# Optimization experiments

Measured on AMD Instinct MI355X. Metric: run time of the kernel, lower is better.

Reference implementation:

```python
import jax, jax.numpy as jnp
import numpy as np

LN_EPS = 1e-5


def _layernorm_c(x, g, b):
    # x: (B, C, H, W); LayerNorm over channel dim (torch permutes to channels-last)
    m = x.mean(axis=1, keepdims=True)
    v = ((x - m) ** 2).mean(axis=1, keepdims=True)
    xn = (x - m) / jnp.sqrt(v + LN_EPS)
    return xn * g[None, :, None, None] + b[None, :, None, None]


def _conv1x1(x, w, b):
    # w: (O, C) equivalent of Conv2d kernel_size=1
    return jnp.einsum('oc,bchw->bohw', w, x) + b[None, :, None, None]


def _rel_indices(lw):
    # matches torch: indices (x,y) for x in range(lw) for y in range(lw);
    # torch indexes the (2*lw-1, 2*lw-1) table with NEGATIVE distances (python wrap),
    # which equals modulo (2*lw-1).
    pos = np.stack(np.meshgrid(np.arange(lw), np.arange(lw), indexing='ij'), -1).reshape(-1, 2)
    rel = (pos[None, :, :] - pos[:, None, :]) % (2 * lw - 1)
    return rel[..., 0], rel[..., 1]


def setup_inputs() -> dict:
    key = jax.random.key(0)
    ks = jax.random.split(key, 8)
    B, N, D, H, DFF, LW = 1, 240, 256, 8, 2048, 20
    src = jax.random.normal(ks[0], (B, D, N, N), dtype=jnp.float32)
    valid = 220  # last window block fully padded -> exercises full-mask reset path
    pad1d = jnp.arange(N) >= valid
    padding_mask = (pad1d[:, None] | pad1d[None, :])[None, None]  # (B,1,N,N) bool
    s = 0.02
    return {
        'src': src,
        'padding_mask': padding_mask,
        'qkv_w': jax.random.normal(ks[1], (3 * D, D), dtype=jnp.float32) * s,
        'qkv_b': jnp.zeros((3 * D,), jnp.float32),
        'out_w': jax.random.normal(ks[2], (D, D), dtype=jnp.float32) * s,
        'out_b': jnp.zeros((D,), jnp.float32),
        'lin1_w': jax.random.normal(ks[3], (DFF, D), dtype=jnp.float32) * s,
        'lin1_b': jnp.zeros((DFF,), jnp.float32),
        'lin2_w': jax.random.normal(ks[4], (D, DFF), dtype=jnp.float32) * s,
        'lin2_b': jnp.zeros((D,), jnp.float32),
        'n1_g': jnp.ones((D,), jnp.float32),
        'n1_b': jnp.zeros((D,), jnp.float32),
        'n2_g': jnp.ones((D,), jnp.float32),
        'n2_b': jnp.zeros((D,), jnp.float32),
        'rel_bias': jax.random.normal(ks[5], (2 * LW - 1, 2 * LW - 1, H), dtype=jnp.float32) * 0.02,
    }


def reference(src, padding_mask, qkv_w, qkv_b, out_w, out_b, lin1_w, lin1_b,
              lin2_w, lin2_b, n1_g, n1_b, n2_g, n2_b, rel_bias):
    B, D, N, _ = src.shape
    H = rel_bias.shape[-1]
    LW = (rel_bias.shape[0] + 1) // 2
    nw = N // LW           # shift_offset=0, N % LW == 0 -> no spatial padding
    F = LW * LW            # eff_attn_field
    hd = D // H
    scaling = float(hd) ** -0.5

    # pre-norm
    src2 = _layernorm_c(src, n1_g, n1_b)

    # window partition: (B,D,N,N) -> (B*nw*nw, D, LW, LW)
    pm = src2.reshape(B, D, nw, LW, nw, LW).transpose(0, 2, 4, 1, 3, 5)
    pm = pm.reshape(B * nw * nw, D, LW, LW)

    # key padding mask per window: (B*nw*nw, F)
    kpm = padding_mask[:, 0].reshape(B, nw, LW, nw, LW).transpose(0, 1, 3, 2, 4)
    kpm = kpm.reshape(B * nw * nw, F)
    full = kpm.all(axis=-1)                      # fully padded windows
    kpm = kpm & (~full)[:, None]                 # index_fill_(False) equivalent

    # qkv (1x1 conv) + heads
    qkv = _conv1x1(pm, qkv_w, qkv_b)             # (eb, 3D, LW, LW)
    q, k, v = jnp.split(qkv, 3, axis=1)
    eb = q.shape[0]
    q = (q * scaling).reshape(eb, H, hd, F)
    k = k.reshape(eb, H, hd, F)
    v = v.reshape(eb, H, hd, F)

    attn = jnp.einsum('bhdi,bhdj->bhij', q, k)   # (eb, H, F, F)
    attn = jnp.where(kpm[:, None, None, :], -jnp.inf, attn)
    r0, r1 = _rel_indices(LW)
    rel = rel_bias[r0, r1]                       # (F, F, H)
    attn = attn + jnp.transpose(rel, (2, 0, 1))[None]
    attn = jax.nn.softmax(attn, axis=-1)

    out = jnp.einsum('bhij,bhdj->bhdi', attn, v).reshape(eb, D, LW, LW)
    out = _conv1x1(out, out_w, out_b)

    # window merge: (B*nw*nw, D, LW, LW) -> (B, D, N, N)
    out = out.reshape(B, nw, nw, D, LW, LW).transpose(0, 3, 1, 4, 2, 5).reshape(B, D, N, N)

    src = src + out  # dropout1 = identity (eval)

    # FFN
    s2 = _layernorm_c(src, n2_g, n2_b)
    s2 = _conv1x1(jax.nn.relu(_conv1x1(s2, lin1_w, lin1_b)), lin2_w, lin2_b)
    src = src + s2   # dropout2 = identity (eval)

    src = jnp.where(padding_mask, 0.0, src)
    return src
```

## Files before the change

kernel.cpp:

```cpp
#include <hip/hip_runtime.h>
#include <hip/hip_bf16.h>
#include <math.h>

typedef unsigned short u16;
typedef unsigned int   u32;
typedef __attribute__((ext_vector_type(8))) short bf16x8;
typedef __attribute__((ext_vector_type(4))) float f32x4;
typedef __attribute__((ext_vector_type(16))) float f32x16;
typedef __attribute__((ext_vector_type(4))) u32 u32x4;

#define NSIDE  240
#define NPIX   57600
#define DMODEL 256
#define NHEAD  8
#define HDIM   32
#define LWIN   20
#define NWIN   12
#define FF     400
#define DFFN   2048
#define BTAB   39
#define LOG2E  1.4426950408889634f
#define QSCALE 0.2550773933046f

#define OFF_QKVW  0u
#define OFF_OUTW  393216u
#define OFF_W1    524288u
#define OFF_W2    1572864u
#define OFF_FLAG  2621440u
#define OFF_WANY  2621504u
#define OFF_WMASK 2622080u
#define OFF_NM    2629568u
#define OFF_A     2687488u
#define OFF_B     32178688u

__device__ __forceinline__ float bf2f(u16 u){
  union { float f; u32 i; } v; v.i = ((u32)u) << 16; return v.f;
}
__device__ __forceinline__ float bflo(u32 u){
  union { float f; u32 i; } v; v.i = u << 16; return v.f;
}
__device__ __forceinline__ float bfhi(u32 u){
  union { float f; u32 i; } v; v.i = u & 0xffff0000u; return v.f;
}
__device__ __forceinline__ u16 f2bf(float f){
  union { float f; u32 i; } v; v.f = f;
  u32 r = v.i + 0x7fffu + ((v.i >> 16) & 1u);
  return (u16)(r >> 16);
}
__device__ __forceinline__ u32 pkbf(float a, float b){
  float2 f2; f2.x = a; f2.y = b;
  __hip_bfloat162 h = __float22bfloat162_rn(f2);
  union { __hip_bfloat162 h; u32 u; } c; c.h = h; return c.u;
}
__device__ __forceinline__ void gload16(const void* g, void* l){
  __builtin_amdgcn_global_load_lds((const __attribute__((address_space(1))) u32*)g,
                                   (__attribute__((address_space(3))) u32*)l, 16, 0, 0);
}
__device__ __forceinline__ void gload16nt(const void* g, void* l){
  __builtin_amdgcn_global_load_lds((const __attribute__((address_space(1))) u32*)g,
                                   (__attribute__((address_space(3))) u32*)l, 16, 0, 2);
}

__global__ void cvt_kernel(const float* __restrict__ in, u16* __restrict__ out, int n){
  int i = blockIdx.x * 256 + threadIdx.x;
  if (i < n) out[i] = f2bf(in[i]);
}
__global__ void cvt_w1T(const float* __restrict__ in, u16* __restrict__ out){
  int i = blockIdx.x * 256 + threadIdx.x;
  int f = i >> 8, k = i & 255;
  int lane = (f & 15) | (((k >> 3) & 3) << 4);
  size_t dst = ((size_t)((f >> 4) * 8 + (k >> 5)) * 64 + lane) * 8 + (k & 7);
  out[dst] = f2bf(in[i]);
}
__global__ void cvt_w2T(const float* __restrict__ in, u16* __restrict__ out){
  int i = blockIdx.x * 256 + threadIdx.x;
  int o = i >> 11, f = i & 2047;
  int lane = (o & 15) | (((f >> 3) & 3) << 4);
  size_t dst = ((size_t)((o >> 4) * 64 + (f >> 5)) * 64 + lane) * 8 + (f & 7);
  out[dst] = f2bf(in[i]);
}

__global__ void zero_flag(int* __restrict__ flag){ *flag = 0; }
__global__ void detect_mask(const unsigned char* __restrict__ m, int* __restrict__ flag){
  int p = blockIdx.x * 256 + threadIdx.x;
  int i = p / NSIDE, j = p - i * NSIDE;
  int a = (m[p] != 0), b = (m[j * NSIDE + i] != 0);
  unsigned long long ball = __ballot(a != b);
  if ((threadIdx.x & 63) == 0 && ball) atomicOr(flag, 1);
}
__global__ void norm_mask(const void* __restrict__ m, const int* __restrict__ flag,
                          unsigned char* __restrict__ nm){
  int p = blockIdx.x * 256 + threadIdx.x;
  int v;
  if (*flag) v = (((const int*)m)[p] != 0);
  else       v = (((const unsigned char*)m)[p] != 0);
  nm[p] = (unsigned char)v;
}

__global__ void wmask_kernel(const unsigned char* __restrict__ nm,
                             u32* __restrict__ wmask, int* __restrict__ wany){
  int w = blockIdx.x;
  int wi = w / NWIN, wj = w % NWIN;
  __shared__ u32 bits[13];
  __shared__ int cnt;
  int t = threadIdx.x;
  if (t < 13) bits[t] = 0;
  if (t == 0) cnt = 0;
  __syncthreads();
  if (t < FF){
    int pj = (wi * LWIN + t / LWIN) * NSIDE + wj * LWIN + (t % LWIN);
    if (nm[pj]){ atomicOr(&bits[t >> 5], 1u << (t & 31)); atomicAdd(&cnt, 1); }
  }
  __syncthreads();
  int full = (cnt == FF);
  if (t < 13) wmask[w * 13 + t] = full ? 0u : bits[t];
  if (t == 0) wany[w] = (cnt > 0 && !full) ? 1 : 0;
}

__global__ __launch_bounds__(256) void ln_kernel(const float* __restrict__ x,
                          const float* __restrict__ g, const float* __restrict__ b,
                          u16* __restrict__ out){
  int p = blockIdx.x * 256 + threadIdx.x;
  float s = 0.f, s2 = 0.f;
  for (int c = 0; c < DMODEL; c++){
    float v = x[c * NPIX + p];
    s += v; s2 += v * v;
  }
  float m = s * (1.f / DMODEL);
  float var = s2 * (1.f / DMODEL) - m * m;
  float inv = rsqrtf(var + 1e-5f);
  u16* orow = out + (size_t)p * DMODEL;
  for (int c0 = 0; c0 < DMODEL; c0 += 8){
    u32 wq[4];
    #pragma unroll
    for (int q = 0; q < 4; q++){
      int c = c0 + 2 * q;
      float v0 = (x[c * NPIX + p] - m) * inv * g[c] + b[c];
      float v1 = (x[(c + 1) * NPIX + p] - m) * inv * g[c + 1] + b[c + 1];
      wq[q] = pkbf(v0, v1);
    }
    uint4 st; st.x = wq[0]; st.y = wq[1]; st.z = wq[2]; st.w = wq[3];
    *(uint4*)&orow[c0] = st;
  }
}

template<int EPI, int XHM>
__global__ __launch_bounds__(256) void gemm_nt(const u16* __restrict__ W,
    const u16* __restrict__ Xt, const float* __restrict__ bias,
    const float* __restrict__ res, void* __restrict__ outp, int M){
  __shared__ u16 SM[128 * 128];
  u16* Ws = SM;
  u16* Xs = SM + 8192;
  int t = threadIdx.x, wv = t >> 6, ln = t & 63;
  int n0 = blockIdx.x * 128, m0 = blockIdx.y * 128;
  int wr = wv >> 1, wc = wv & 1;
  f32x4 acc[4][4];
  #pragma unroll
  for (int r = 0; r < 4; r++)
    #pragma unroll
    for (int c = 0; c < 4; c++) acc[r][c] = (f32x4)0.f;
  const char* Wb = (const char*)W;
  const char* Xb = (const char*)Xt;
  for (int k0 = 0; k0 < 256; k0 += 64){
    #pragma unroll
    for (int i = 0; i < 4; i++){
      int cb = i * 256 + wv * 64;
      int idx = cb + ln;
      int row = idx >> 3, cc = idx & 7;
      int cc2 = cc ^ (row & 7);
      gload16(Wb + (size_t)(m0 + row) * 512 + k0 * 2 + (cc2 << 4), (char*)Ws + cb * 16);
      if (XHM){
        int head = (k0 >> 5) + (cc2 >> 2);
        gload16(Xb + ((size_t)head * NPIX + n0 + row) * 64 + ((cc2 & 3) << 4),
                (char*)Xs + cb * 16);
      } else {
        gload16(Xb + (size_t)(n0 + row) * 512 + k0 * 2 + (cc2 << 4), (char*)Xs + cb * 16);
      }
    }
    __syncthreads();
    #pragma unroll
    for (int kk = 0; kk < 64; kk += 32){
      int kidx = kk + (ln >> 4) * 8;
      int swz = (ln & 7) << 3;
      bf16x8 af[4], bfr[4];
      #pragma unroll
      for (int r = 0; r < 4; r++){
        int row = wr * 64 + r * 16 + (ln & 15);
        af[r] = *(const bf16x8*)&Ws[row * 64 + (kidx ^ swz)];
      }
      #pragma unroll
      for (int c = 0; c < 4; c++){
        int row = wc * 64 + c * 16 + (ln & 15);
        bfr[c] = *(const bf16x8*)&Xs[row * 64 + (kidx ^ swz)];
      }
      #pragma unroll
      for (int r = 0; r < 4; r++)
        #pragma unroll
        for (int c = 0; c < 4; c++)
          acc[r][c] = __builtin_amdgcn_mfma_f32_16x16x32_bf16(af[r], bfr[c], acc[r][c], 0, 0, 0);
    }
    __syncthreads();
  }
  if (EPI == 2){
    float sc = (m0 < 256) ? QSCALE : 1.0f;
    #pragma unroll
    for (int r = 0; r < 4; r++){
      int mo0 = wr * 64 + r * 16 + (ln >> 4) * 4;
      f32x4 bv = *(const f32x4*)&bias[m0 + mo0];
      #pragma unroll
      for (int c = 0; c < 4; c++){
        int no = wc * 64 + c * 16 + (ln & 15);
        uint2 pk;
        pk.x = pkbf((acc[r][c][0] + bv[0]) * sc, (acc[r][c][1] + bv[1]) * sc);
        pk.y = pkbf((acc[r][c][2] + bv[2]) * sc, (acc[r][c][3] + bv[3]) * sc);
        *(uint2*)&SM[no * 128 + mo0] = pk;
      }
    }
    __syncthreads();
    u16* ob = (u16*)outp;
    int plane8 = (m0 >> 8) * 8 + ((m0 & 255) >> 5);
    #pragma unroll
    for (int it = 0; it < 8; it++){
      int idx = t + it * 256;
      int pr = idx >> 4, ch = idx & 15;
      int hl = ch >> 2;
      int off = (ch & 3) * 8;
      uint4 v = *(const uint4*)&SM[pr * 128 + ch * 8];
      *(uint4*)&ob[((size_t)(plane8 + hl) * NPIX + n0 + pr) * 32 + off] = v;
    }
  } else {
    #pragma unroll
    for (int r = 0; r < 4; r++){
      int mo0 = m0 + wr * 64 + r * 16 + (ln >> 4) * 4;
      f32x4 bv = *(const f32x4*)&bias[mo0];
      #pragma unroll
      for (int c = 0; c < 4; c++){
        int no = n0 + wc * 64 + c * 16 + (ln & 15);
        #pragma unroll
        for (int q = 0; q < 4; q++){
          float v = acc[r][c][q] + bv[q];
          size_t oi = (size_t)(mo0 + q) * NPIX + no;
          ((float*)outp)[oi] = v + res[oi];
        }
      }
    }
  }
}

__global__ __launch_bounds__(256, 2) void attn_kernel(
    const u16* __restrict__ qkvP, const float* __restrict__ relb,
    const u32* __restrict__ wmask, const int* __restrict__ wany,
    u16* __restrict__ out)
{
  __shared__ u16 Ks[400 * 32];
  __shared__ u16 Vs[32 * 420];
  __shared__ float bs[BTAB * BTAB];
  int bid = blockIdx.x;
  int h = bid & 7, w = bid >> 3;
  int wi = w / NWIN, wj = w % NWIN;
  int t = threadIdx.x, wv = t >> 6, ln = t & 63;
  const char* kpl = (const char*)qkvP + (size_t)(8 + h) * NPIX * 64;
  const u16*  vpl = qkvP + (size_t)(16 + h) * NPIX * 32;
  const u16*  qpl = qkvP + (size_t)h * NPIX * 32;
  for (int e = t; e < BTAB * BTAB; e += 256){
    int a = e / BTAB, b = e - a * BTAB;
    int r0 = a + 20; if (r0 >= BTAB) r0 -= BTAB;
    int r1 = b + 20; if (r1 >= BTAB) r1 -= BTAB;
    bs[e] = LOG2E * relb[(r0 * BTAB + r1) * NHEAD + h];
  }
  #pragma unroll
  for (int it = 0; it < 7; it++){
    int base = it * 256 + wv * 64;
    if (base < 1600){
      int idx = base + ln;
      int j = idx >> 2, c = idx & 3;
      int pj = (wi * LWIN + j / LWIN) * NSIDE + wj * LWIN + (j % LWIN);
      gload16nt(kpl + (size_t)pj * 64 + ((c ^ (j & 3)) << 4), (char*)Ks + base * 16);
    }
  }
  for (int it = 0; it < 7; it++){
    int idx = t + it * 256;
    int j = idx >> 2, c = idx & 3;
    if (j >= 416) break;
    int d0 = c * 8;
    if (j < FF){
      int pj = (wi * LWIN + j / LWIN) * NSIDE + wj * LWIN + (j % LWIN);
      u32x4 vv = __builtin_nontemporal_load((const u32x4*)&vpl[(size_t)pj * 32 + c * 8]);
      #pragma unroll
      for (int q = 0; q < 4; q++){
        Vs[(d0 + 2 * q) * 420 + j]     = (u16)vv[q];
        Vs[(d0 + 2 * q + 1) * 420 + j] = (u16)(vv[q] >> 16);
      }
    } else {
      #pragma unroll
      for (int q = 0; q < 4; q++){
        Vs[(d0 + 2 * q) * 420 + j]     = 0;
        Vs[(d0 + 2 * q + 1) * 420 + j] = 0;
      }
    }
  }
  __syncthreads();
  int lane31 = ln & 31, hi = ln >> 5;
  int anym = wany[w];
  for (int it8 = wv; it8 < 13; it8 += 4){
    int i = it8 * 32 + lane31;
    int ic = i < FF ? i : FF - 1;
    int xi = ic / LWIN, yi = ic - xi * LWIN;
    int pi = (wi * LWIN + xi) * NSIDE + wj * LWIN + yi;
    int Coff = (19 - xi) * BTAB + (19 - yi);
    bf16x8 qf0 = __builtin_nontemporal_load((const bf16x8*)&qpl[(size_t)pi * 32 + hi * 8]);
    bf16x8 qf1 = __builtin_nontemporal_load((const bf16x8*)&qpl[(size_t)pi * 32 + 16 + hi * 8]);
    float m = -3e38f, lsum = 0.f;
    f32x16 o;
    #pragma unroll
    for (int r = 0; r < 16; r++) o[r] = 0.f;
    for (int jt = 0; jt < 13; jt++){
      f32x16 acc;
      int jbase = jt * 32 + 4 * hi;
      #pragma unroll
      for (int r = 0; r < 16; r++){
        int j = jbase + (r & 3) + 8 * (r >> 2);
        int jc2 = j < FF ? j : 0;
        int xj = jc2 / LWIN;
        int yj = jc2 - xj * LWIN;
        float bv = bs[xj * BTAB + yj + Coff];
        acc[r] = (j < FF) ? bv : -1e30f;
      }
      int jb0 = jt * 32 + lane31;
      int jrc = jb0 < FF ? jb0 : FF - 1;
      const char* kb = (const char*)Ks + jrc * 64;
      bf16x8 kf0 = *(const bf16x8*)(kb + ((hi ^ (jrc & 3)) << 4));
      bf16x8 kf1 = *(const bf16x8*)(kb + (((2 + hi) ^ (jrc & 3)) << 4));
      acc = __builtin_amdgcn_mfma_f32_32x32x16_bf16(kf0, qf0, acc, 0, 0, 0);
      acc = __builtin_amdgcn_mfma_f32_32x32x16_bf16(kf1, qf1, acc, 0, 0, 0);
      if (anym){
        u32 mb = wmask[w * 13 + jt];
        if (mb){
          #pragma unroll
          for (int r = 0; r < 16; r++){
            int jb = (r & 3) + 8 * (r >> 2) + 4 * hi;
            if ((mb >> jb) & 1) acc[r] = -1e30f;
          }
        }
      }
      float tm = acc[0];
      #pragma unroll
      for (int r = 1; r < 16; r++) tm = fmaxf(tm, acc[r]);
      tm = fmaxf(tm, __shfl_xor(tm, 32));
      if (tm > m + 6.f){
        float sc = exp2f(m - tm);
        lsum *= sc;
        #pragma unroll
        for (int r = 0; r < 16; r++) o[r] *= sc;
        m = tm;
      }
      float ls = 0.f;
      #pragma unroll
      for (int r = 0; r < 16; r++){ float pv = exp2f(acc[r] - m); acc[r] = pv; ls += pv; }
      lsum += ls;
      u32 x01 = pkbf(acc[0], acc[1]), x23 = pkbf(acc[2], acc[3]);
      u32 x45 = pkbf(acc[4], acc[5]), x67 = pkbf(acc[6], acc[7]);
      u32 y01 = __shfl_xor(x01, 32), y23 = __shfl_xor(x23, 32);
      u32 y45 = __shfl_xor(x45, 32), y67 = __shfl_xor(x67, 32);
      union { u32 u[4]; bf16x8 v; } f0;
      f0.u[0] = hi ? y45 : x01; f0.u[1] = hi ? y67 : x23;
      f0.u[2] = hi ? x45 : y01; f0.u[3] = hi ? x67 : y23;
      bf16x8 vf0 = *(const bf16x8*)&Vs[lane31 * 420 + jt * 32 + hi * 8];
      o = __builtin_amdgcn_mfma_f32_32x32x16_bf16(vf0, f0.v, o, 0, 0, 0);
      if (jt < 12){
        u32 x89 = pkbf(acc[8], acc[9]),   xab = pkbf(acc[10], acc[11]);
        u32 xcd2 = pkbf(acc[12], acc[13]), xef = pkbf(acc[14], acc[15]);
        u32 y89 = __shfl_xor(x89, 32), yab = __shfl_xor(xab, 32);
        u32 ycd = __shfl_xor(xcd2, 32), yef = __shfl_xor(xef, 32);
        union { u32 u[4]; bf16x8 v; } f1;
        f1.u[0] = hi ? ycd : x89; f1.u[1] = hi ? yef : xab;
        f1.u[2] = hi ? xcd2 : y89; f1.u[3] = hi ? xef : yab;
        bf16x8 vf1 = *(const bf16x8*)&Vs[lane31 * 420 + jt * 32 + 16 + hi * 8];
        o = __builtin_amdgcn_mfma_f32_32x32x16_bf16(vf1, f1.v, o, 0, 0, 0);
      }
    }
    lsum += __shfl_xor(lsum, 32);
    if (i < FF){
      float linv = 1.f / lsum;
      u16* orow = out + ((size_t)h * NPIX + pi) * 32;
      #pragma unroll
      for (int g = 0; g < 4; g++){
        int ch0 = g * 8 + hi * 4;
        uint2 st;
        st.x = pkbf(o[g * 4 + 0] * linv, o[g * 4 + 1] * linv);
        st.y = pkbf(o[g * 4 + 2] * linv, o[g * 4 + 3] * linv);
        *(uint2*)&orow[ch0] = st;
      }
    }
  }
}

__global__ __launch_bounds__(256, 3) void ffn_kernel(const u16* __restrict__ xt,
    const u16* __restrict__ w1T, const u16* __restrict__ w2T,
    const float* __restrict__ b1, const float* __restrict__ b2,
    const float* __restrict__ resid, const unsigned char* __restrict__ pmask,
    float* __restrict__ out){
  __shared__ u16 Xs[64 * 256];
  __shared__ u16 Hs[64 * 136];
  int t = threadIdx.x, wv = t >> 6, ln = t & 63;
  int q4 = ln >> 4, l15 = ln & 15;
  int p0 = blockIdx.x * 64;
  const char* xb = (const char*)xt + (size_t)p0 * 512;
  #pragma unroll
  for (int it = 0; it < 8; it++){
    int cb = it * 256 + wv * 64;
    int idx = cb + ln;
    int row = idx >> 5, cc = idx & 31;
    gload16(xb + row * 512 + ((cc << 4) ^ ((row & 7) << 4)), (char*)Xs + cb * 16);
  }
  f32x4 acc[4][4];
  #pragma unroll
  for (int r = 0; r < 4; r++)
    #pragma unroll
    for (int c = 0; c < 4; c++) acc[r][c] = (f32x4)0.f;
  int swx = (ln & 7) << 3;
  __syncthreads();
  for (int fc = 0; fc < DFFN; fc += 128){
    f32x4 ha[2][4];
    #pragma unroll
    for (int ft = 0; ft < 2; ft++)
      #pragma unroll
      for (int c = 0; c < 4; c++) ha[ft][c] = (f32x4)0.f;
    const u16* w1f = w1T + ((size_t)((fc >> 4) + wv * 2) * 8 * 64 + ln) * 8;
    #pragma unroll
    for (int kg = 0; kg < 8; kg++){
      bf16x8 aw0 = *(const bf16x8*)(w1f + (size_t)kg * 512);
      bf16x8 aw1 = *(const bf16x8*)(w1f + (size_t)(8 + kg) * 512);
      #pragma unroll
      for (int c = 0; c < 4; c++){
        int p = c * 16 + l15;
        bf16x8 bx = *(const bf16x8*)&Xs[p * 256 + ((kg * 32 + q4 * 8) ^ swx)];
        ha[0][c] = __builtin_amdgcn_mfma_f32_16x16x32_bf16(aw0, bx, ha[0][c], 0, 0, 0);
        ha[1][c] = __builtin_amdgcn_mfma_f32_16x16x32_bf16(aw1, bx, ha[1][c], 0, 0, 0);
      }
    }
    __syncthreads();
    #pragma unroll
    for (int ft = 0; ft < 2; ft++){
      int f0 = wv * 32 + ft * 16 + q4 * 4;
      f32x4 bv1 = *(const f32x4*)&b1[fc + f0];
      #pragma unroll
      for (int c = 0; c < 4; c++){
        int p = c * 16 + l15;
        uint2 pk;
        pk.x = pkbf(fmaxf(ha[ft][c][0] + bv1[0], 0.f), fmaxf(ha[ft][c][1] + bv1[1], 0.f));
        pk.y = pkbf(fmaxf(ha[ft][c][2] + bv1[2], 0.f), fmaxf(ha[ft][c][3] + bv1[3], 0.f));
        *(uint2*)&Hs[p * 136 + f0] = pk;
      }
    }
    __syncthreads();
    #pragma unroll
    for (int kk2 = 0; kk2 < 4; kk2++){
      bf16x8 a2[4], hb[4];
      #pragma unroll
      for (int r = 0; r < 4; r++)
        a2[r] = *(const bf16x8*)(w2T + ((size_t)((wv * 4 + r) * 64 + (fc >> 5) + kk2) * 64 + ln) * 8);
      #pragma unroll
      for (int c = 0; c < 4; c++)
        hb[c] = *(const bf16x8*)&Hs[(c * 16 + l15) * 136 + kk2 * 32 + q4 * 8];
      #pragma unroll
      for (int r = 0; r < 4; r++)
        #pragma unroll
        for (int c = 0; c < 4; c++)
          acc[r][c] = __builtin_amdgcn_mfma_f32_16x16x32_bf16(a2[r], hb[c], acc[r][c], 0, 0, 0);
    }
  }
  #pragma unroll
  for (int r = 0; r < 4; r++){
    int o0 = wv * 64 + r * 16 + q4 * 4;
    f32x4 bv = *(const f32x4*)&b2[o0];
    #pragma unroll
    for (int c = 0; c < 4; c++){
      int p = p0 + c * 16 + l15;
      int msk = pmask[p];
      #pragma unroll
      for (int q = 0; q < 4; q++){
        size_t oi = (size_t)(o0 + q) * NPIX + p;
        float v = acc[r][c][q] + bv[q] + resid[oi];
        out[oi] = msk ? 0.f : v;
      }
    }
  }
}

extern "C" void kernel_launch(void* const* d_in, const int* in_sizes, int n_in,
                              void* d_out, int out_size, void* d_ws, size_t ws_size,
                              hipStream_t stream){
  const float* src    = (const float*)d_in[0];
  const void*  pmraw  = d_in[1];
  const float* qkv_w  = (const float*)d_in[2];
  const float* qkv_b  = (const float*)d_in[3];
  const float* out_w  = (const float*)d_in[4];
  const float* out_b  = (const float*)d_in[5];
  const float* lin1_w = (const float*)d_in[6];
  const float* lin1_b = (const float*)d_in[7];
  const float* lin2_w = (const float*)d_in[8];
  const float* lin2_b = (const float*)d_in[9];
  const float* n1_g   = (const float*)d_in[10];
  const float* n1_b   = (const float*)d_in[11];
  const float* n2_g   = (const float*)d_in[12];
  const float* n2_b   = (const float*)d_in[13];
  const float* relb   = (const float*)d_in[14];

  char* ws = (char*)d_ws;
  u16* qkvw_bf = (u16*)(ws + OFF_QKVW);
  u16* outw_bf = (u16*)(ws + OFF_OUTW);
  u16* w1_fr   = (u16*)(ws + OFF_W1);
  u16* w2_fr   = (u16*)(ws + OFF_W2);
  int* flag    = (int*)(ws + OFF_FLAG);
  int* wany    = (int*)(ws + OFF_WANY);
  u32* wmaskp  = (u32*)(ws + OFF_WMASK);
  unsigned char* nm = (unsigned char*)(ws + OFF_NM);
  u16* bufA    = (u16*)(ws + OFF_A);
  u16* qkvP    = (u16*)(ws + OFF_B);
  float* x1    = (float*)(ws + OFF_B);

  cvt_kernel<<<768,  256, 0, stream>>>(qkv_w,  qkvw_bf, 768 * 256);
  cvt_kernel<<<256,  256, 0, stream>>>(out_w,  outw_bf, 256 * 256);
  cvt_w1T<<<2048, 256, 0, stream>>>(lin1_w, w1_fr);
  cvt_w2T<<<2048, 256, 0, stream>>>(lin2_w, w2_fr);
  zero_flag<<<1, 1, 0, stream>>>(flag);
  detect_mask<<<225, 256, 0, stream>>>((const unsigned char*)pmraw, flag);
  norm_mask<<<225, 256, 0, stream>>>(pmraw, flag, nm);
  wmask_kernel<<<144, 512, 0, stream>>>(nm, wmaskp, wany);

  ln_kernel<<<225, 256, 0, stream>>>(src, n1_g, n1_b, bufA);
  gemm_nt<2, 0><<<dim3(450, 6), 256, 0, stream>>>(qkvw_bf, bufA, qkv_b, nullptr,
                                                  (void*)qkvP, 768);
  attn_kernel<<<1152, 256, 0, stream>>>(qkvP, relb, wmaskp, wany, bufA);
  gemm_nt<1, 1><<<dim3(450, 2), 256, 0, stream>>>(outw_bf, bufA, out_b, src,
                                                  (void*)x1, 256);
  ln_kernel<<<225, 256, 0, stream>>>(x1, n2_g, n2_b, bufA);
  ffn_kernel<<<900, 256, 0, stream>>>(bufA, w1_fr, w2_fr, lin1_b, lin2_b, x1, nm,
                                      (float*)d_out);
}
```

Before: 550.8 us.

## Keep FFN input in registers and double-buffer hidden tile to drop a barrier

The first FFN GEMM now has each wave own a 16-pixel slice and hold its X fragments in registers. Each wave computes all 128 hidden features for its pixels, where before each wave computed 32 features across all 64 pixels. The shared-memory arena is reused: X is staged once, then the space becomes a double-buffered hidden tile, so one __syncthreads per chunk is removed and LDS use drops. In exchange, every wave now reads the whole 128-feature W1 chunk from global memory (four times the per-wave weight traffic), and register pressure rises.

```diff
diff --git a/kernel.cpp b/kernel.cpp
--- a/kernel.cpp
+++ b/kernel.cpp
@@ -21,6 +21,7 @@
 #define BTAB   39
 #define LOG2E  1.4426950408889634f
 #define QSCALE 0.2550773933046f
+#define HSTR   136
 
 #define OFF_QKVW  0u
 #define OFF_OUTW  393216u
@@ -400,8 +401,7 @@
     const float* __restrict__ b1, const float* __restrict__ b2,
     const float* __restrict__ resid, const unsigned char* __restrict__ pmask,
     float* __restrict__ out){
-  __shared__ u16 Xs[64 * 256];
-  __shared__ u16 Hs[64 * 136];
+  __shared__ u16 SM[17408];
   int t = threadIdx.x, wv = t >> 6, ln = t & 63;
   int q4 = ln >> 4, l15 = ln & 15;
   int p0 = blockIdx.x * 64;
@@ -411,47 +411,44 @@
     int cb = it * 256 + wv * 64;
     int idx = cb + ln;
     int row = idx >> 5, cc = idx & 31;
-    gload16(xb + row * 512 + ((cc << 4) ^ ((row & 7) << 4)), (char*)Xs + cb * 16);
-  }
+    gload16(xb + row * 512 + ((cc << 4) ^ ((row & 7) << 4)), (char*)SM + cb * 16);
+  }
+  __syncthreads();
+  int swx = (ln & 7) << 3;
+  bf16x8 bxr[8];
+  #pragma unroll
+  for (int kg = 0; kg < 8; kg++)
+    bxr[kg] = *(const bf16x8*)&SM[(wv * 16 + l15) * 256 + ((kg * 32 + q4 * 8) ^ swx)];
   f32x4 acc[4][4];
   #pragma unroll
   for (int r = 0; r < 4; r++)
     #pragma unroll
     for (int c = 0; c < 4; c++) acc[r][c] = (f32x4)0.f;
-  int swx = (ln & 7) << 3;
   __syncthreads();
-  for (int fc = 0; fc < DFFN; fc += 128){
-    f32x4 ha[2][4];
-    #pragma unroll
-    for (int ft = 0; ft < 2; ft++)
-      #pragma unroll
-      for (int c = 0; c < 4; c++) ha[ft][c] = (f32x4)0.f;
-    const u16* w1f = w1T + ((size_t)((fc >> 4) + wv * 2) * 8 * 64 + ln) * 8;
+  int cur = 0;
+  for (int fc = 0; fc < DFFN; fc += 128, cur ^= 1){
+    u16* Hc = SM + cur * 8704;
+    f32x4 ha[8];
+    #pragma unroll
+    for (int ft = 0; ft < 8; ft++) ha[ft] = (f32x4)0.f;
+    const u16* w1f = w1T + ((size_t)(fc >> 4) * 512 + ln) * 8;
     #pragma unroll
     for (int kg = 0; kg < 8; kg++){
-      bf16x8 aw0 = *(const bf16x8*)(w1f + (size_t)kg * 512);
-      bf16x8 aw1 = *(const bf16x8*)(w1f + (size_t)(8 + kg) * 512);
-      #pragma unroll
-      for (int c = 0; c < 4; c++){
-        int p = c * 16 + l15;
-        bf16x8 bx = *(const bf16x8*)&Xs[p * 256 + ((kg * 32 + q4 * 8) ^ swx)];
-        ha[0][c] = __builtin_amdgcn_mfma_f32_16x16x32_bf16(aw0, bx, ha[0][c], 0, 0, 0);
-        ha[1][c] = __builtin_amdgcn_mfma_f32_16x16x32_bf16(aw1, bx, ha[1][c], 0, 0, 0);
-      }
-    }
-    __syncthreads();
-    #pragma unroll
-    for (int ft = 0; ft < 2; ft++){
-      int f0 = wv * 32 + ft * 16 + q4 * 4;
+      bf16x8 bx = bxr[kg];
+      #pragma unroll
+      for (int ft = 0; ft < 8; ft++){
+        bf16x8 aw = *(const bf16x8*)(w1f + (size_t)(ft * 4096 + kg * 512));
+        ha[ft] = __builtin_amdgcn_mfma_f32_16x16x32_bf16(aw, bx, ha[ft], 0, 0, 0);
+      }
+    }
+    #pragma unroll
+    for (int ft = 0; ft < 8; ft++){
+      int f0 = ft * 16 + q4 * 4;
       f32x4 bv1 = *(const f32x4*)&b1[fc + f0];
-      #pragma unroll
-      for (int c = 0; c < 4; c++){
-        int p = c * 16 + l15;
-        uint2 pk;
-        pk.x = pkbf(fmaxf(ha[ft][c][0] + bv1[0], 0.f), fmaxf(ha[ft][c][1] + bv1[1], 0.f));
-        pk.y = pkbf(fmaxf(ha[ft][c][2] + bv1[2], 0.f), fmaxf(ha[ft][c][3] + bv1[3], 0.f));
-        *(uint2*)&Hs[p * 136 + f0] = pk;
-      }
+      uint2 pk;
+      pk.x = pkbf(fmaxf(ha[ft][0] + bv1[0], 0.f), fmaxf(ha[ft][1] + bv1[1], 0.f));
+      pk.y = pkbf(fmaxf(ha[ft][2] + bv1[2], 0.f), fmaxf(ha[ft][3] + bv1[3], 0.f));
+      *(uint2*)&Hc[(wv * 16 + l15) * HSTR + f0] = pk;
     }
     __syncthreads();
     #pragma unroll
@@ -462,7 +459,7 @@
         a2[r] = *(const bf16x8*)(w2T + ((size_t)((wv * 4 + r) * 64 + (fc >> 5) + kk2) * 64 + ln) * 8);
       #pragma unroll
       for (int c = 0; c < 4; c++)
-        hb[c] = *(const bf16x8*)&Hs[(c * 16 + l15) * 136 + kk2 * 32 + q4 * 8];
+        hb[c] = *(const bf16x8*)&Hc[(c * 16 + l15) * HSTR + kk2 * 32 + q4 * 8];
       #pragma unroll
       for (int r = 0; r < 4; r++)
         #pragma unroll
```

After: 987.3 us. +79.2%, slower.
